# Performance work log

Hardware: AMD Instinct MI355X
Metric: run time of the kernel (lower is better)

The kernel has to match this reference:

```python
import jax, jax.numpy as jnp
import numpy as np

B, S, WIDTH, M = 2, 240, 128, 20
PAD = 16


def setup_inputs() -> dict:
    key = jax.random.key(0)
    ks = jax.random.split(key, 10)
    scale = 1.0 / (WIDTH * WIDTH)
    inp = {
        "x": jax.random.normal(ks[0], (B, S, S, 3), jnp.float32),
        "fc0_w": jax.random.normal(ks[1], (5, WIDTH), jnp.float32) * 0.1,
        "fc0_b": jnp.zeros((WIDTH,), jnp.float32),
        # 5 spectral layers, complex weights stored as [..., 2] = (real, imag)
        "spec_w1": jax.random.uniform(ks[2], (5, WIDTH, WIDTH, M, M, 2), jnp.float32) * scale,
        "spec_w2": jax.random.uniform(ks[3], (5, WIDTH, WIDTH, M, M, 2), jnp.float32) * scale,
        # 5 residual 1x1 convs
        "w_w": jax.random.normal(ks[4], (5, WIDTH, WIDTH), jnp.float32) / np.sqrt(WIDTH),
        "w_b": jnp.zeros((5, WIDTH), jnp.float32),
        "fc1_w": jax.random.normal(ks[5], (WIDTH, WIDTH), jnp.float32) / np.sqrt(WIDTH),
        "fc1_b": jnp.zeros((WIDTH,), jnp.float32),
        # 4 heads (u, v, p, T): width->64->1
        "head1_w": jax.random.normal(ks[6], (4, WIDTH, 64), jnp.float32) / np.sqrt(WIDTH),
        "head1_b": jnp.zeros((4, 64), jnp.float32),
        "head2_w": jax.random.normal(ks[7], (4, 64, 1), jnp.float32) / 8.0,
        "head2_b": jnp.zeros((4, 1), jnp.float32),
    }
    return inp


def _spectral_conv(h, w1, w2):
    # h: (B, C, H, W) real; w1, w2: (C_in, C_out, M, M) complex64
    Hh, Ww = h.shape[-2], h.shape[-1]
    ft = jnp.fft.rfft2(h)  # (B, C, H, W//2+1)
    o1 = jnp.einsum('bixy,ioxy->boxy', ft[:, :, :M, :M], w1)
    o2 = jnp.einsum('bixy,ioxy->boxy', ft[:, :, -M:, :M], w2)
    out_ft = jnp.zeros((h.shape[0], w1.shape[1], Hh, Ww // 2 + 1), jnp.complex64)
    out_ft = out_ft.at[:, :, :M, :M].set(o1).at[:, :, -M:, :M].set(o2)
    return jnp.fft.irfft2(out_ft, s=(Hh, Ww))


def reference(x, fc0_w, fc0_b, spec_w1, spec_w2, w_w, w_b, fc1_w, fc1_b,
              head1_w, head1_b, head2_w, head2_b):
    Bn, sx, sy = x.shape[0], x.shape[1], x.shape[2]
    gx = jnp.broadcast_to(jnp.linspace(0.0, 1.0, sx, dtype=x.dtype)[None, :, None, None], (Bn, sx, sy, 1))
    gy = jnp.broadcast_to(jnp.linspace(0.0, 1.0, sy, dtype=x.dtype)[None, None, :, None], (Bn, sx, sy, 1))
    x1 = jnp.concatenate([x, gx, gy], axis=-1)          # (B, S, S, 5)
    h = x1 @ fc0_w + fc0_b                              # lift -> (B, S, S, width)
    h = jnp.transpose(h, (0, 3, 1, 2))                  # (B, width, S, S)
    h = jnp.pad(h, ((0, 0), (0, 0), (0, PAD), (0, PAD)))
    c1 = spec_w1[..., 0] + 1j * spec_w1[..., 1]
    c2 = spec_w2[..., 0] + 1j * spec_w2[..., 1]
    for i in range(5):
        s = _spectral_conv(h, c1[i], c2[i])
        lin = jnp.einsum('bchw,oc->bohw', h, w_w[i]) + w_b[i][None, :, None, None]
        h = s + lin
        if i < 4:
            h = jax.nn.gelu(h, approximate=False)
    h = h[..., :-PAD, :-PAD]
    h = jnp.transpose(h, (0, 2, 3, 1))                  # (B, S, S, width)
    h = jax.nn.gelu(h @ fc1_w + fc1_b, approximate=False)
    h1 = jax.nn.gelu(jnp.einsum('bhwc,kcd->kbhwd', h, head1_w)
                     + head1_b[:, None, None, None, :], approximate=False)
    out = jnp.einsum('kbhwd,kdo->kbhwo', h1, head2_w) + head2_b[:, None, None, None, :]
    return (out[0], out[1], out[2], out[3])  # u, v, p, T each (B, S, S, 1)
```

## Files before the change

kernel.cpp:

```cpp
#include <hip/hip_runtime.h>
#include <math.h>


#define SZ_H   (2ull*256*256*128)
#define O_HA   0ull
#define O_HB   (O_HA + SZ_H)
#define O_G    (O_HB + SZ_H)
#define SZ_G   (2ull*256*20*128*2)
#define O_FTT  (O_G + SZ_G)
#define SZ_FT  (2ull*40*20*128*2)
#define O_OFT  (O_FTT + SZ_FT)
#define O_EY   (O_OFT + SZ_FT)
#define SZ_EY  (256ull*20*2)
#define O_EX   (O_EY + SZ_EY)
#define SZ_EX  (256ull*40*2)
#define O_EXI  (O_EX + SZ_EX)
#define O_WWT  (O_EXI + SZ_EX)
#define SZ_WWT 81920ull
#define O_PART (O_WWT + SZ_WWT)
#define SZ_PART (8ull*204800*2)

static __device__ __forceinline__ float gelu_f(float v) {
    return 0.5f * v * (1.0f + erff(v * 0.70710678118654752f));
}

__global__ void k_prep(const float* __restrict__ w_w, float* __restrict__ ws) {
    int i = blockIdx.x * 256 + threadIdx.x;
    const float STEP = 6.2831853071795864769f / 256.0f;
    if (i < 5120) {
        int ky = i % 20, y = i / 20;
        int t = (ky * y) & 255;
        float th = t * STEP;
        ws[O_EY + 2*(size_t)i]     = cosf(th);
        ws[O_EY + 2*(size_t)i + 1] = -sinf(th);
    } else if (i < 15360) {
        int m = i - 5120; int j = m % 40, x = m / 40;
        int kx = (j < 20) ? j : (216 + j);
        int t = (kx * x) & 255;
        float th = t * STEP;
        ws[O_EX + 2*(size_t)m]     = cosf(th);
        ws[O_EX + 2*(size_t)m + 1] = -sinf(th);
    } else if (i < 25600) {
        int m = i - 15360; int j = m % 40, x = m / 40;
        int kx = (j < 20) ? j : (216 + j);
        int t = (kx * x) & 255;
        float th = t * STEP;
        ws[O_EXI + 2*(size_t)m]     = cosf(th);
        ws[O_EXI + 2*(size_t)m + 1] = sinf(th);
    } else {
        int m = i - 25600;
        if (m < 81920) {
            int l = m >> 14, r = m & 16383;
            int ic = r >> 7, oc = r & 127;
            ws[O_WWT + m] = w_w[(size_t)l*16384 + oc*128 + ic];
        }
    }
}

__global__ __launch_bounds__(256) void k_fc0(const float* __restrict__ xin,
        const float* __restrict__ w, const float* __restrict__ bv,
        float4* __restrict__ H4) {
    size_t e = (size_t)blockIdx.x * 256 + threadIdx.x;
    int c4 = (int)(e & 31) * 4;
    int y = (int)((e >> 5) & 255);
    int x = (int)((e >> 13) & 255);
    int b = (int)(e >> 21);
    float4 h = make_float4(0.f, 0.f, 0.f, 0.f);
    if (x < 240 && y < 240) {
        const float* xp = xin + (((size_t)(b*240 + x))*240 + y)*3;
        float x0 = xp[0], x1 = xp[1], x2 = xp[2];
        float gx = x*(1.0f/239.0f), gy = y*(1.0f/239.0f);
        float4 w0 = *(const float4*)&w[c4];
        float4 w1 = *(const float4*)&w[128 + c4];
        float4 w2 = *(const float4*)&w[256 + c4];
        float4 w3 = *(const float4*)&w[384 + c4];
        float4 w4 = *(const float4*)&w[512 + c4];
        float4 bb = *(const float4*)&bv[c4];
        h.x = bb.x + x0*w0.x + x1*w1.x + x2*w2.x + gx*w3.x + gy*w4.x;
        h.y = bb.y + x0*w0.y + x1*w1.y + x2*w2.y + gx*w3.y + gy*w4.y;
        h.z = bb.z + x0*w0.z + x1*w1.z + x2*w2.z + gx*w3.z + gy*w4.z;
        h.w = bb.w + x0*w0.w + x1*w1.w + x2*w2.w + gx*w3.w + gy*w4.w;
    }
    H4[e] = h;
}

__global__ __launch_bounds__(256) void k_ydft(const float* __restrict__ H,
        const float* __restrict__ Ey, float2* __restrict__ G) {
    int b = blockIdx.x >> 8, x = blockIdx.x & 255;
    int c = threadIdx.x & 127;
    int yq = __builtin_amdgcn_readfirstlane((int)(threadIdx.x >> 7));
    const float* Hrow = H + ((size_t)(b*256 + x)) * 256 * 128;
    float ar[20], ai[20];
    #pragma unroll
    for (int k = 0; k < 20; k++) { ar[k] = 0.f; ai[k] = 0.f; }
    for (int i = 0; i < 128; i++) {
        int y = yq*128 + i;
        float v = Hrow[(size_t)y*128 + c];
        const float* e = Ey + (size_t)y*40;
        #pragma unroll
        for (int k = 0; k < 20; k++) {
            ar[k] = fmaf(v, e[2*k],   ar[k]);
            ai[k] = fmaf(v, e[2*k+1], ai[k]);
        }
    }
    __shared__ float red[20][128][2];
    if (yq == 1) {
        #pragma unroll
        for (int k = 0; k < 20; k++) { red[k][c][0] = ar[k]; red[k][c][1] = ai[k]; }
    }
    __syncthreads();
    if (yq == 0) {
        float2* Gp = G + ((size_t)(b*256 + x))*20*128;
        #pragma unroll
        for (int k = 0; k < 20; k++)
            Gp[k*128 + c] = make_float2(ar[k] + red[k][c][0], ai[k] + red[k][c][1]);
    }
}

__global__ __launch_bounds__(512) void k_xdft(const float2* __restrict__ G,
        const float* __restrict__ Ex, float2* __restrict__ ftT) {
    int t = blockIdx.x;
    int ch = t & 1, jq = (t >> 1) & 1, ky = (t >> 2) % 20, b = t / 80;
    int cl = threadIdx.x & 63;
    int xq = __builtin_amdgcn_readfirstlane((int)(threadIdx.x >> 6));
    int c = ch*64 + cl;
    int j0 = jq * 20;
    float ar[20], ai[20];
    #pragma unroll
    for (int k = 0; k < 20; k++) { ar[k] = 0.f; ai[k] = 0.f; }
    for (int i = 0; i < 32; i++) {
        int x = xq*32 + i;
        float2 g = G[(((size_t)(b*256 + x))*20 + ky)*128 + c];
        const float* e = Ex + (size_t)x*80 + j0*2;
        #pragma unroll
        for (int k = 0; k < 20; k++) {
            float er = e[2*k], ei = e[2*k+1];
            ar[k] = fmaf(g.x, er, fmaf(-g.y, ei, ar[k]));
            ai[k] = fmaf(g.x, ei, fmaf( g.y, er, ai[k]));
        }
    }
    __shared__ float red[4][20][64][2];
    if (xq >= 4) {
        int s = xq - 4;
        #pragma unroll
        for (int k = 0; k < 20; k++) { red[s][k][cl][0] = ar[k]; red[s][k][cl][1] = ai[k]; }
    }
    __syncthreads();
    if (xq < 4) {
        #pragma unroll
        for (int k = 0; k < 20; k++) { ar[k] += red[xq][k][cl][0]; ai[k] += red[xq][k][cl][1]; }
    }
    __syncthreads();
    if (xq == 2 || xq == 3) {
        int s = xq - 2;
        #pragma unroll
        for (int k = 0; k < 20; k++) { red[s][k][cl][0] = ar[k]; red[s][k][cl][1] = ai[k]; }
    }
    __syncthreads();
    if (xq < 2) {
        #pragma unroll
        for (int k = 0; k < 20; k++) { ar[k] += red[xq][k][cl][0]; ai[k] += red[xq][k][cl][1]; }
    }
    __syncthreads();
    if (xq == 1) {
        #pragma unroll
        for (int k = 0; k < 20; k++) { red[0][k][cl][0] = ar[k]; red[0][k][cl][1] = ai[k]; }
    }
    __syncthreads();
    if (xq == 0) {
        #pragma unroll
        for (int k = 0; k < 20; k++) {
            float rr = ar[k] + red[0][k][cl][0];
            float ii = ai[k] + red[0][k][cl][1];
            ftT[((size_t)c*2 + b)*800 + (size_t)(j0 + k)*20 + ky] = make_float2(rr, ii);
        }
    }
}

__global__ __launch_bounds__(448) void k_modemix(const float2* __restrict__ w1,
        const float2* __restrict__ w2, const float2* __restrict__ ftT,
        float2* __restrict__ outp, int ic_per) {
    int bid = blockIdx.x & 255;
    int icq = blockIdx.x >> 8;
    int oc = bid >> 1;
    int mh = bid & 1;
    int tid = threadIdx.x;
    if (tid >= 400) return;
    int wsel = tid / 200;
    int m = mh*200 + (tid % 200);
    int jk = wsel*400 + m;
    const float2* wb = wsel ? w2 : w1;
    int ic0 = icq * ic_per;
    float ar0=0.f, ai0=0.f, ar1=0.f, ai1=0.f;
    #pragma unroll 4
    for (int i = 0; i < ic_per; i++) {
        int ic = ic0 + i;
        float2 wv = wb[((size_t)(ic*128 + oc))*400 + m];
        float2 f0 = ftT[(size_t)ic*1600 + jk];
        float2 f1 = ftT[(size_t)ic*1600 + 800 + jk];
        ar0 = fmaf(f0.x, wv.x, fmaf(-f0.y, wv.y, ar0));
        ai0 = fmaf(f0.x, wv.y, fmaf( f0.y, wv.x, ai0));
        ar1 = fmaf(f1.x, wv.x, fmaf(-f1.y, wv.y, ar1));
        ai1 = fmaf(f1.x, wv.y, fmaf( f1.y, wv.x, ai1));
    }
    float2* o = outp + (size_t)icq * 204800;
    o[(size_t)jk*128 + oc]         = make_float2(ar0, ai0);
    o[(size_t)(800 + jk)*128 + oc] = make_float2(ar1, ai1);
}

__global__ __launch_bounds__(512) void k_modered(const float2* __restrict__ part,
        float2* __restrict__ oft) {
    int i = blockIdx.x * 512 + threadIdx.x;
    if (i >= 204800) return;
    float2 s = part[i];
    #pragma unroll
    for (int q = 1; q < 8; q++) {
        float2 p = part[(size_t)q*204800 + i];
        s.x += p.x; s.y += p.y;
    }
    oft[i] = s;
}

__global__ __launch_bounds__(256) void k_xidft(const float2* __restrict__ oft,
        const float* __restrict__ Exi, float2* __restrict__ T) {
    int b = blockIdx.x >> 7, xq = blockIdx.x & 127;
    int oc = threadIdx.x & 127;
    int xs = __builtin_amdgcn_readfirstlane((int)(threadIdx.x >> 7));
    int x = xq*2 + xs;
    float ar[20], ai[20];
    #pragma unroll
    for (int k = 0; k < 20; k++) { ar[k] = 0.f; ai[k] = 0.f; }
    const float2* ob = oft + (size_t)b*800*128;
    for (int j = 0; j < 40; j++) {
        float er = Exi[(size_t)x*80 + 2*j], ei = Exi[(size_t)x*80 + 2*j + 1];
        #pragma unroll
        for (int k = 0; k < 20; k++) {
            float2 o = ob[(size_t)(j*20 + k)*128 + oc];
            ar[k] = fmaf(o.x, er, fmaf(-o.y, ei, ar[k]));
            ai[k] = fmaf(o.x, ei, fmaf( o.y, er, ai[k]));
        }
    }
    float2* Tp = T + ((size_t)(b*256 + x))*20*128;
    #pragma unroll
    for (int k = 0; k < 20; k++) Tp[k*128 + oc] = make_float2(ar[k], ai[k]);
}

__global__ __launch_bounds__(256) void k_spec_lin(const float* __restrict__ H,
        const float2* __restrict__ T, const float* __restrict__ wwT,
        const float* __restrict__ wb, float* __restrict__ Hout, int do_gelu) {
    int yg = blockIdx.x & 3;
    int x  = (blockIdx.x >> 2) & 255;
    int b  = blockIdx.x >> 10;
    int tid = threadIdx.x;
    int ocg = tid & 31;
    int ys  = tid >> 5;
    __shared__ float  Hl[64][128];
    __shared__ float2 Tl[128][22];
    __shared__ float2 trig[20][64];
    int y0 = yg*64;
    const float* Hbase = H + (((size_t)(b*256 + x))*256 + y0)*128;
    #pragma unroll
    for (int it = 0; it < 8; it++) {
        int i = tid + it*256;
        int pi = i >> 5, c4 = (i & 31)*4;
        *(float4*)&Hl[pi][c4] = *(const float4*)&Hbase[(size_t)pi*128 + c4];
    }
    const float2* Tp = T + ((size_t)(b*256 + x))*20*128;
    for (int i = tid; i < 2560; i += 256) Tl[i & 127][i >> 7] = Tp[i];
    for (int i = tid; i < 1280; i += 256) {
        int ky = i >> 6, yl = i & 63;
        int t = (ky * (y0 + yl)) & 255;
        float th = t * (6.2831853071795864769f/256.0f);
        float f = (ky == 0 ? 1.0f : 2.0f) * (1.0f/65536.0f);
        trig[ky][yl] = make_float2(f*cosf(th), f*sinf(th));
    }
    __syncthreads();
    int oc0 = ocg*4;
    float acc[4][8];
    #pragma unroll
    for (int q = 0; q < 4; q++)
        #pragma unroll
        for (int yy = 0; yy < 8; yy++) acc[q][yy] = 0.f;
    for (int icc = 0; icc < 32; icc++) {
        float4 hv[8];
        #pragma unroll
        for (int p = 0; p < 8; p++) hv[p] = *(float4*)&Hl[ys*8 + p][icc*4];
        float4 wA = *(const float4*)&wwT[(size_t)(icc*4+0)*128 + oc0];
        float4 wB = *(const float4*)&wwT[(size_t)(icc*4+1)*128 + oc0];
        float4 wC = *(const float4*)&wwT[(size_t)(icc*4+2)*128 + oc0];
        float4 wD = *(const float4*)&wwT[(size_t)(icc*4+3)*128 + oc0];
        #pragma unroll
        for (int p = 0; p < 8; p++) {
            float4 h4 = hv[p];
            acc[0][p] = fmaf(h4.x, wA.x, fmaf(h4.y, wB.x, fmaf(h4.z, wC.x, fmaf(h4.w, wD.x, acc[0][p]))));
            acc[1][p] = fmaf(h4.x, wA.y, fmaf(h4.y, wB.y, fmaf(h4.z, wC.y, fmaf(h4.w, wD.y, acc[1][p]))));
            acc[2][p] = fmaf(h4.x, wA.z, fmaf(h4.y, wB.z, fmaf(h4.z, wC.z, fmaf(h4.w, wD.z, acc[2][p]))));
            acc[3][p] = fmaf(h4.x, wA.w, fmaf(h4.y, wB.w, fmaf(h4.z, wC.w, fmaf(h4.w, wD.w, acc[3][p]))));
        }
    }
    #pragma unroll
    for (int ky = 0; ky < 20; ky++) {
        float2 t0 = Tl[oc0+0][ky], t1 = Tl[oc0+1][ky];
        float2 t2 = Tl[oc0+2][ky], t3 = Tl[oc0+3][ky];
        #pragma unroll
        for (int yy = 0; yy < 8; yy++) {
            float2 cs = trig[ky][ys*8+yy];
            acc[0][yy] = fmaf(t0.x, cs.x, fmaf(-t0.y, cs.y, acc[0][yy]));
            acc[1][yy] = fmaf(t1.x, cs.x, fmaf(-t1.y, cs.y, acc[1][yy]));
            acc[2][yy] = fmaf(t2.x, cs.x, fmaf(-t2.y, cs.y, acc[2][yy]));
            acc[3][yy] = fmaf(t3.x, cs.x, fmaf(-t3.y, cs.y, acc[3][yy]));
        }
    }
    float4 bb = *(const float4*)&wb[oc0];
    #pragma unroll
    for (int yy = 0; yy < 8; yy++) {
        float4 o;
        o.x = acc[0][yy] + bb.x; o.y = acc[1][yy] + bb.y;
        o.z = acc[2][yy] + bb.z; o.w = acc[3][yy] + bb.w;
        if (do_gelu) { o.x = gelu_f(o.x); o.y = gelu_f(o.y); o.z = gelu_f(o.z); o.w = gelu_f(o.w); }
        *(float4*)&Hout[(((size_t)(b*256 + x))*256 + y0 + ys*8 + yy)*128 + oc0] = o;
    }
}

__global__ __launch_bounds__(256) void k_head(const float* __restrict__ H,
        const float* __restrict__ fc1_w, const float* __restrict__ fc1_b,
        const float* __restrict__ h1w, const float* __restrict__ h1b,
        const float* __restrict__ h2w, const float* __restrict__ h2b,
        float* __restrict__ out) {
    int tid = threadIdx.x;
    int p0 = blockIdx.x * 64;
    __shared__ float hl[64][128];
    __shared__ float tl[128][65];
    #pragma unroll
    for (int it = 0; it < 8; it++) {
        int i = tid + it*256;
        int pi = i >> 5, c4 = (i & 31)*4;
        int p = p0 + pi;
        int b = p / 57600, r = p % 57600;
        int xx = r / 240, yy = r % 240;
        *(float4*)&hl[pi][c4] = *(const float4*)&H[(((size_t)(b*256 + xx))*256 + yy)*128 + c4];
    }
    __syncthreads();
    {
        int ocg = tid & 31, pxg = tid >> 5;
        int oc0 = ocg*4, px0 = pxg*8;
        float acc[4][8];
        #pragma unroll
        for (int q = 0; q < 4; q++)
            #pragma unroll
            for (int p = 0; p < 8; p++) acc[q][p] = 0.f;
        for (int icc = 0; icc < 32; icc++) {
            float4 hv[8];
            #pragma unroll
            for (int p = 0; p < 8; p++) hv[p] = *(float4*)&hl[px0 + p][icc*4];
            float4 wA = *(const float4*)&fc1_w[(size_t)(icc*4+0)*128 + oc0];
            float4 wB = *(const float4*)&fc1_w[(size_t)(icc*4+1)*128 + oc0];
            float4 wC = *(const float4*)&fc1_w[(size_t)(icc*4+2)*128 + oc0];
            float4 wD = *(const float4*)&fc1_w[(size_t)(icc*4+3)*128 + oc0];
            #pragma unroll
            for (int p = 0; p < 8; p++) {
                float4 h4 = hv[p];
                acc[0][p] = fmaf(h4.x, wA.x, fmaf(h4.y, wB.x, fmaf(h4.z, wC.x, fmaf(h4.w, wD.x, acc[0][p]))));
                acc[1][p] = fmaf(h4.x, wA.y, fmaf(h4.y, wB.y, fmaf(h4.z, wC.y, fmaf(h4.w, wD.y, acc[1][p]))));
                acc[2][p] = fmaf(h4.x, wA.z, fmaf(h4.y, wB.z, fmaf(h4.z, wC.z, fmaf(h4.w, wD.z, acc[2][p]))));
                acc[3][p] = fmaf(h4.x, wA.w, fmaf(h4.y, wB.w, fmaf(h4.z, wC.w, fmaf(h4.w, wD.w, acc[3][p]))));
            }
        }
        float4 bb = *(const float4*)&fc1_b[oc0];
        float bq[4] = {bb.x, bb.y, bb.z, bb.w};
        #pragma unroll
        for (int q = 0; q < 4; q++)
            #pragma unroll
            for (int p = 0; p < 8; p++)
                tl[oc0 + q][px0 + p] = gelu_f(acc[q][p] + bq[q]);
    }
    __syncthreads();
    {
        int k = tid >> 6, dg = tid & 15, pxg = (tid >> 4) & 3;
        int d0 = dg*4, px0 = pxg*16;
        float acc2[4][16];
        #pragma unroll
        for (int q = 0; q < 4; q++)
            #pragma unroll
            for (int i = 0; i < 16; i++) acc2[q][i] = 0.f;
        const float* wp = h1w + (size_t)k*8192 + d0;
        for (int c = 0; c < 128; c++) {
            float4 w = *(const float4*)&wp[(size_t)c*64];
            #pragma unroll
            for (int i = 0; i < 16; i++) {
                float v = tl[c][px0 + i];
                acc2[0][i] = fmaf(v, w.x, acc2[0][i]);
                acc2[1][i] = fmaf(v, w.y, acc2[1][i]);
                acc2[2][i] = fmaf(v, w.z, acc2[2][i]);
                acc2[3][i] = fmaf(v, w.w, acc2[3][i]);
            }
        }
        float4 b1 = *(const float4*)&h1b[k*64 + d0];
        float4 w2 = *(const float4*)&h2w[k*64 + d0];
        float ob = h2b[k];
        #pragma unroll
        for (int i = 0; i < 16; i++) {
            float u = gelu_f(acc2[0][i] + b1.x) * w2.x
                    + gelu_f(acc2[1][i] + b1.y) * w2.y
                    + gelu_f(acc2[2][i] + b1.z) * w2.z
                    + gelu_f(acc2[3][i] + b1.w) * w2.w;
            u += __shfl_down(u, 8);
            u += __shfl_down(u, 4);
            u += __shfl_down(u, 2);
            u += __shfl_down(u, 1);
            if (dg == 0) out[(size_t)k*115200 + p0 + px0 + i] = u + ob;
        }
    }
}

extern "C" void kernel_launch(void* const* d_in, const int* in_sizes, int n_in,
                              void* d_out, int out_size, void* d_ws, size_t ws_size,
                              hipStream_t stream) {
    const float* x       = (const float*)d_in[0];
    const float* fc0_w   = (const float*)d_in[1];
    const float* fc0_b   = (const float*)d_in[2];
    const float* spec_w1 = (const float*)d_in[3];
    const float* spec_w2 = (const float*)d_in[4];
    const float* w_w     = (const float*)d_in[5];
    const float* w_b     = (const float*)d_in[6];
    const float* fc1_w   = (const float*)d_in[7];
    const float* fc1_b   = (const float*)d_in[8];
    const float* head1_w = (const float*)d_in[9];
    const float* head1_b = (const float*)d_in[10];
    const float* head2_w = (const float*)d_in[11];
    const float* head2_b = (const float*)d_in[12];
    float* ws = (float*)d_ws;
    float* out = (float*)d_out;

    int split = ws_size >= (size_t)(O_PART + SZ_PART) * 4 ? 1 : 0;

    k_prep<<<420, 256, 0, stream>>>(w_w, ws);
    k_fc0<<<16384, 256, 0, stream>>>(x, fc0_w, fc0_b, (float4*)(ws + O_HA));

    float* cur = ws + O_HA;
    float* nxt = ws + O_HB;
    float2* G    = (float2*)(ws + O_G);
    float2* ftT  = (float2*)(ws + O_FTT);
    float2* oft  = (float2*)(ws + O_OFT);
    float2* part = (float2*)(ws + O_PART);

    for (int l = 0; l < 5; l++) {
        k_ydft<<<512, 256, 0, stream>>>(cur, ws + O_EY, G);
        k_xdft<<<160, 512, 0, stream>>>(G, ws + O_EX, ftT);
        const float2* w1l = (const float2*)(spec_w1 + (size_t)l*13107200);
        const float2* w2l = (const float2*)(spec_w2 + (size_t)l*13107200);
        if (split) {
            k_modemix<<<2048, 448, 0, stream>>>(w1l, w2l, ftT, part, 16);
            k_modered<<<400, 512, 0, stream>>>(part, oft);
        } else {
            k_modemix<<<256, 448, 0, stream>>>(w1l, w2l, ftT, oft, 128);
        }
        k_xidft<<<256, 256, 0, stream>>>(oft, ws + O_EXI, G);
        k_spec_lin<<<2048, 256, 0, stream>>>(cur, G, ws + O_WWT + (size_t)l*16384,
                                             w_b + l*128, nxt, (l < 4) ? 1 : 0);
        float* t = cur; cur = nxt; nxt = t;
    }
    k_head<<<1800, 256, 0, stream>>>(cur, fc1_w, fc1_b, head1_w, head1_b,
                                     head2_w, head2_b, out);
}
```

Baseline: 2.088 ms.

## Restructure spectral-linear kernel per-lane points and split head into fc1 and heads kernels

```diff
diff --git a/kernel.cpp b/kernel.cpp
--- a/kernel.cpp
+++ b/kernel.cpp
@@ -19,6 +19,7 @@
 #define SZ_WWT 81920ull
 #define O_PART (O_WWT + SZ_WWT)
 #define SZ_PART (8ull*204800*2)
+#define FC1_B_NEED (O_G + 6356992ull)
 
 static __device__ __forceinline__ float gelu_f(float v) {
     return 0.5f * v * (1.0f + erff(v * 0.70710678118654752f));
@@ -252,74 +253,167 @@
     int x  = (blockIdx.x >> 2) & 255;
     int b  = blockIdx.x >> 10;
     int tid = threadIdx.x;
-    int ocg = tid & 31;
-    int ys  = tid >> 5;
-    __shared__ float  Hl[64][128];
-    __shared__ float2 Tl[128][22];
-    __shared__ float2 trig[20][64];
-    int y0 = yg*64;
+    int lane = tid & 63;
+    int wv = __builtin_amdgcn_readfirstlane(tid >> 6);
+    int oc0 = wv * 32;
+    int y0 = yg * 64;
+    __shared__ float hl[64][129];
     const float* Hbase = H + (((size_t)(b*256 + x))*256 + y0)*128;
     #pragma unroll
     for (int it = 0; it < 8; it++) {
         int i = tid + it*256;
         int pi = i >> 5, c4 = (i & 31)*4;
-        *(float4*)&Hl[pi][c4] = *(const float4*)&Hbase[(size_t)pi*128 + c4];
-    }
-    const float2* Tp = T + ((size_t)(b*256 + x))*20*128;
-    for (int i = tid; i < 2560; i += 256) Tl[i & 127][i >> 7] = Tp[i];
-    for (int i = tid; i < 1280; i += 256) {
-        int ky = i >> 6, yl = i & 63;
-        int t = (ky * (y0 + yl)) & 255;
-        float th = t * (6.2831853071795864769f/256.0f);
-        float f = (ky == 0 ? 1.0f : 2.0f) * (1.0f/65536.0f);
-        trig[ky][yl] = make_float2(f*cosf(th), f*sinf(th));
-    }
-    __syncthreads();
-    int oc0 = ocg*4;
-    float acc[4][8];
-    #pragma unroll
-    for (int q = 0; q < 4; q++)
-        #pragma unroll
-        for (int yy = 0; yy < 8; yy++) acc[q][yy] = 0.f;
-    for (int icc = 0; icc < 32; icc++) {
-        float4 hv[8];
-        #pragma unroll
-        for (int p = 0; p < 8; p++) hv[p] = *(float4*)&Hl[ys*8 + p][icc*4];
-        float4 wA = *(const float4*)&wwT[(size_t)(icc*4+0)*128 + oc0];
-        float4 wB = *(const float4*)&wwT[(size_t)(icc*4+1)*128 + oc0];
-        float4 wC = *(const float4*)&wwT[(size_t)(icc*4+2)*128 + oc0];
-        float4 wD = *(const float4*)&wwT[(size_t)(icc*4+3)*128 + oc0];
-        #pragma unroll
-        for (int p = 0; p < 8; p++) {
-            float4 h4 = hv[p];
-            acc[0][p] = fmaf(h4.x, wA.x, fmaf(h4.y, wB.x, fmaf(h4.z, wC.x, fmaf(h4.w, wD.x, acc[0][p]))));
-            acc[1][p] = fmaf(h4.x, wA.y, fmaf(h4.y, wB.y, fmaf(h4.z, wC.y, fmaf(h4.w, wD.y, acc[1][p]))));
-            acc[2][p] = fmaf(h4.x, wA.z, fmaf(h4.y, wB.z, fmaf(h4.z, wC.z, fmaf(h4.w, wD.z, acc[2][p]))));
-            acc[3][p] = fmaf(h4.x, wA.w, fmaf(h4.y, wB.w, fmaf(h4.z, wC.w, fmaf(h4.w, wD.w, acc[3][p]))));
-        }
-    }
-    #pragma unroll
-    for (int ky = 0; ky < 20; ky++) {
-        float2 t0 = Tl[oc0+0][ky], t1 = Tl[oc0+1][ky];
-        float2 t2 = Tl[oc0+2][ky], t3 = Tl[oc0+3][ky];
-        #pragma unroll
-        for (int yy = 0; yy < 8; yy++) {
-            float2 cs = trig[ky][ys*8+yy];
-            acc[0][yy] = fmaf(t0.x, cs.x, fmaf(-t0.y, cs.y, acc[0][yy]));
-            acc[1][yy] = fmaf(t1.x, cs.x, fmaf(-t1.y, cs.y, acc[1][yy]));
-            acc[2][yy] = fmaf(t2.x, cs.x, fmaf(-t2.y, cs.y, acc[2][yy]));
-            acc[3][yy] = fmaf(t3.x, cs.x, fmaf(-t3.y, cs.y, acc[3][yy]));
-        }
-    }
-    float4 bb = *(const float4*)&wb[oc0];
-    #pragma unroll
-    for (int yy = 0; yy < 8; yy++) {
-        float4 o;
-        o.x = acc[0][yy] + bb.x; o.y = acc[1][yy] + bb.y;
-        o.z = acc[2][yy] + bb.z; o.w = acc[3][yy] + bb.w;
-        if (do_gelu) { o.x = gelu_f(o.x); o.y = gelu_f(o.y); o.z = gelu_f(o.z); o.w = gelu_f(o.w); }
-        *(float4*)&Hout[(((size_t)(b*256 + x))*256 + y0 + ys*8 + yy)*128 + oc0] = o;
-    }
+        float4 v = *(const float4*)&Hbase[(size_t)pi*128 + c4];
+        hl[pi][c4] = v.x; hl[pi][c4+1] = v.y; hl[pi][c4+2] = v.z; hl[pi][c4+3] = v.w;
+    }
+    float csr[20], csi[20];
+    {
+        int y = y0 + lane;
+        #pragma unroll
+        for (int k = 0; k < 20; k++) {
+            int t = (k * y) & 255;
+            float th = t * (6.2831853071795864769f/256.0f);
+            float f = (k == 0 ? 1.0f : 2.0f) * (1.0f/65536.0f);
+            csr[k] = f * __cosf(th);
+            csi[k] = f * __sinf(th);
+        }
+    }
+    __syncthreads();
+    float acc[32];
+    #pragma unroll
+    for (int o = 0; o < 32; o++) acc[o] = 0.f;
+    for (int ic = 0; ic < 128; ic++) {
+        float t = hl[lane][ic];
+        const float* wr = &wwT[(size_t)ic*128 + oc0];
+        #pragma unroll
+        for (int o4 = 0; o4 < 8; o4++) {
+            float4 w = *(const float4*)&wr[o4*4];
+            acc[o4*4]   = fmaf(t, w.x, acc[o4*4]);
+            acc[o4*4+1] = fmaf(t, w.y, acc[o4*4+1]);
+            acc[o4*4+2] = fmaf(t, w.z, acc[o4*4+2]);
+            acc[o4*4+3] = fmaf(t, w.w, acc[o4*4+3]);
+        }
+    }
+    const float2* Tp = T + ((size_t)(b*256 + x))*20*128 + oc0;
+    for (int k = 0; k < 20; k++) {
+        const float2* tr = Tp + (size_t)k*128;
+        float cr = csr[k], ci = csi[k];
+        #pragma unroll
+        for (int o = 0; o < 32; o++) {
+            float2 tv = tr[o];
+            acc[o] = fmaf(tv.x, cr, fmaf(-tv.y, ci, acc[o]));
+        }
+    }
+    __syncthreads();
+    const float* bp = &wb[oc0];
+    #pragma unroll
+    for (int o = 0; o < 32; o++) {
+        float v = acc[o] + bp[o];
+        if (do_gelu) v = gelu_f(v);
+        hl[lane][oc0 + o] = v;
+    }
+    __syncthreads();
+    float* Obase = Hout + (((size_t)(b*256 + x))*256 + y0)*128;
+    #pragma unroll
+    for (int it = 0; it < 32; it++) {
+        int i = tid + it*256;
+        int pi = i >> 7, c = i & 127;
+        Obase[(size_t)pi*128 + c] = hl[pi][c];
+    }
+}
+
+__global__ __launch_bounds__(128) void k_fc1(const float* __restrict__ H,
+        const float* __restrict__ fc1_w, const float* __restrict__ fc1_b,
+        float* __restrict__ outA, float* __restrict__ outB) {
+    int tid = threadIdx.x;
+    int lane = tid & 63;
+    int wv = __builtin_amdgcn_readfirstlane(tid >> 6);
+    int p0 = blockIdx.x * 64;
+    __shared__ float hl[64][129];
+    #pragma unroll
+    for (int it = 0; it < 16; it++) {
+        int i = tid + it*128;
+        int pi = i >> 5, c4 = (i & 31)*4;
+        int p = p0 + pi;
+        int bb = p / 57600, r = p % 57600;
+        int xx = r / 240, yy = r % 240;
+        float4 v = *(const float4*)&H[(((size_t)(bb*256 + xx))*256 + yy)*128 + c4];
+        hl[pi][c4] = v.x; hl[pi][c4+1] = v.y; hl[pi][c4+2] = v.z; hl[pi][c4+3] = v.w;
+    }
+    __syncthreads();
+    int oc0 = wv*64;
+    float acc[64];
+    #pragma unroll
+    for (int o = 0; o < 64; o++) acc[o] = 0.f;
+    for (int ic = 0; ic < 128; ic++) {
+        float t = hl[lane][ic];
+        const float* wr = &fc1_w[(size_t)ic*128 + oc0];
+        #pragma unroll
+        for (int o4 = 0; o4 < 16; o4++) {
+            float4 w = *(const float4*)&wr[o4*4];
+            acc[o4*4]   = fmaf(t, w.x, acc[o4*4]);
+            acc[o4*4+1] = fmaf(t, w.y, acc[o4*4+1]);
+            acc[o4*4+2] = fmaf(t, w.z, acc[o4*4+2]);
+            acc[o4*4+3] = fmaf(t, w.w, acc[o4*4+3]);
+        }
+    }
+    __syncthreads();
+    const float* bp = &fc1_b[oc0];
+    #pragma unroll
+    for (int o = 0; o < 64; o++) hl[lane][oc0 + o] = gelu_f(acc[o] + bp[o]);
+    __syncthreads();
+    float* outp = (p0 < 65536) ? (outA + (size_t)p0*128)
+                               : (outB + ((size_t)(p0 - 65536))*128);
+    #pragma unroll
+    for (int it = 0; it < 64; it++) {
+        int i = tid + it*128;
+        int pi = i >> 7, c = i & 127;
+        outp[(size_t)pi*128 + c] = hl[pi][c];
+    }
+}
+
+__global__ __launch_bounds__(256) void k_heads(const float* __restrict__ inA,
+        const float* __restrict__ inB, const float* __restrict__ h1w,
+        const float* __restrict__ h1b, const float* __restrict__ h2w,
+        const float* __restrict__ h2b, float* __restrict__ out) {
+    int tid = threadIdx.x;
+    int lane = tid & 63;
+    int k = __builtin_amdgcn_readfirstlane(tid >> 6);
+    int p0 = blockIdx.x * 64;
+    __shared__ float tl[128][65];
+    const float* inp = (p0 < 65536) ? (inA + (size_t)p0*128)
+                                    : (inB + ((size_t)(p0 - 65536))*128);
+    #pragma unroll
+    for (int it = 0; it < 8; it++) {
+        int i = tid + it*256;
+        int pi = i >> 5, c4 = (i & 31)*4;
+        float4 v = *(const float4*)&inp[(size_t)pi*128 + c4];
+        tl[c4][pi] = v.x; tl[c4+1][pi] = v.y; tl[c4+2][pi] = v.z; tl[c4+3][pi] = v.w;
+    }
+    __syncthreads();
+    float acc[64];
+    #pragma unroll
+    for (int d = 0; d < 64; d++) acc[d] = 0.f;
+    const float* wk = h1w + (size_t)k*8192;
+    for (int c = 0; c < 128; c++) {
+        float t = tl[c][lane];
+        const float* wr = &wk[c*64];
+        #pragma unroll
+        for (int d4 = 0; d4 < 16; d4++) {
+            float4 w = *(const float4*)&wr[d4*4];
+            acc[d4*4]   = fmaf(t, w.x, acc[d4*4]);
+            acc[d4*4+1] = fmaf(t, w.y, acc[d4*4+1]);
+            acc[d4*4+2] = fmaf(t, w.z, acc[d4*4+2]);
+            acc[d4*4+3] = fmaf(t, w.w, acc[d4*4+3]);
+        }
+    }
+    const float* b1 = &h1b[k*64];
+    const float* w2 = &h2w[k*64];
+    float res = 0.f;
+    #pragma unroll
+    for (int d = 0; d < 64; d++)
+        res += gelu_f(acc[d] + b1[d]) * w2[d];
+    out[(size_t)k*115200 + p0 + lane] = res + h2b[k];
 }
 
 __global__ __launch_bounds__(256) void k_head(const float* __restrict__ H,
@@ -432,7 +526,8 @@
     float* ws = (float*)d_ws;
     float* out = (float*)d_out;
 
-    int split = ws_size >= (size_t)(O_PART + SZ_PART) * 4 ? 1 : 0;
+    int split      = ws_size >= (size_t)(O_PART + SZ_PART) * 4 ? 1 : 0;
+    int head_split = ws_size >= (size_t)FC1_B_NEED * 4 ? 1 : 0;
 
     k_prep<<<420, 256, 0, stream>>>(w_w, ws);
     k_fc0<<<16384, 256, 0, stream>>>(x, fc0_w, fc0_b, (float4*)(ws + O_HA));
@@ -460,6 +555,14 @@
                                              w_b + l*128, nxt, (l < 4) ? 1 : 0);
         float* t = cur; cur = nxt; nxt = t;
     }
-    k_head<<<1800, 256, 0, stream>>>(cur, fc1_w, fc1_b, head1_w, head1_b,
-                                     head2_w, head2_b, out);
-}
+    if (head_split) {
+        float* fA = ws + O_HA;
+        float* fB = ws + O_G;
+        k_fc1<<<1800, 128, 0, stream>>>(cur, fc1_w, fc1_b, fA, fB);
+        k_heads<<<1800, 256, 0, stream>>>(fA, fB, head1_w, head1_b,
+                                          head2_w, head2_b, out);
+    } else {
+        k_head<<<1800, 256, 0, stream>>>(cur, fc1_w, fc1_b, head1_w, head1_b,
+                                         head2_w, head2_b, out);
+    }
+}
```

After: 1.959 ms. -6.2%, faster.
